# Performance work log

Hardware: AMD Instinct MI355X
Metric: run time of the kernel (lower is better)

The kernel has to match this reference:

```python
import jax, jax.numpy as jnp
import numpy as np

NO_LANE = 90  # sentinel label meaning 'no lane'

def smooth_l1(x):
    ax = jnp.abs(x)
    return jnp.where(ax < 1.0, 0.5 * x * x, ax - 0.5)

def setup_inputs() -> dict:
    key = jax.random.key(0)
    ks = jax.random.split(key, 10)
    B, M, T, L, NL, P = 32768, 6, 30, 10, 10, 50
    cls_ = jax.random.normal(ks[0], (B, M), dtype=jnp.float32)
    reg = jax.random.normal(ks[1], (B, M, T, 2), dtype=jnp.float32) * 5.0
    lane_cls = jax.random.normal(ks[2], (B, L), dtype=jnp.float32)
    gt_preds = jax.random.normal(ks[3], (B, T, 2), dtype=jnp.float32) * 5.0
    rot = jax.random.normal(ks[4], (B, 2, 2), dtype=jnp.float32)
    orig = jax.random.normal(ks[5], (B, 2), dtype=jnp.float32)
    lane_feats = jax.random.normal(ks[6], (B, NL, P, 2), dtype=jnp.float32) * 5.0
    has_preds = jax.random.uniform(ks[7], (B, T)) < 0.8
    has_preds = has_preds.at[:, 0].set(True)  # ensure mask = max_last > 1.0 holds for every row
    lane_labels = jax.random.randint(ks[8], (B,), 0, L, dtype=jnp.int32)
    lane_labels = jnp.where(jax.random.uniform(ks[9], (B,)) < 0.05, NO_LANE, lane_labels)
    return dict(cls=cls_, reg=reg, lane_cls=lane_cls, gt_preds=gt_preds, rot=rot,
                orig=orig, lane_feats=lane_feats, has_preds=has_preds, lane_labels=lane_labels)

def reference(cls, reg, lane_cls, gt_preds, rot, orig, lane_feats, has_preds, lane_labels):
    B, M, T, _ = reg.shape
    rows = jnp.arange(B)
    hasf = has_preds.astype(jnp.float32)

    # last valid timestep per agent (argmax of has + tiny time ramp)
    last = hasf + 0.1 * jnp.arange(T, dtype=jnp.float32) / T
    last_idcs = jnp.argmax(last, axis=1)
    mask = jnp.max(last, axis=1) > 1.0  # [B], all True by construction
    maskf = mask.astype(jnp.float32)

    # endpoint distance per mode -> min mode selection
    end_reg = reg[rows, :, last_idcs]            # [B, M, 2]
    end_gt = gt_preds[rows, last_idcs]           # [B, 2]
    dist = jnp.sqrt(((end_reg - end_gt[:, None, :]) ** 2).sum(-1))  # [B, M]
    min_idcs = jnp.argmin(dist, axis=1)

    # classification target: mode with min total squared error
    cls_tar = jnp.argmin(((reg - gt_preds[:, None]) ** 2).sum(-1).sum(-1), axis=1)
    nll = -jnp.take_along_axis(jax.nn.log_softmax(cls, axis=-1), cls_tar[:, None], axis=1)[:, 0]
    cls_loss = (nll * maskf).sum() / jnp.maximum(maskf.sum(), 1.0)  # CE mean over masked rows

    reg_sel = reg[rows, min_idcs]                # [B, T, 2]
    w_reg = hasf * maskf[:, None]
    reg_loss = (smooth_l1(reg_sel - gt_preds) * w_reg[:, :, None]).sum()
    num_reg = w_reg.sum()

    # lane classification: per-sample CE * (label+1), skipping sentinel
    valid = lane_labels != NO_LANE
    validf = valid.astype(jnp.float32)
    lab_c = jnp.where(valid, lane_labels, 0)
    lane_nll = -jnp.take_along_axis(jax.nn.log_softmax(lane_cls, axis=-1), lab_c[:, None], axis=1)[:, 0]
    lane_cls_loss = (lane_nll * (lab_c.astype(jnp.float32) + 1.0) * validf).sum()
    num_lane_cls = validf.sum()

    # lane-offset loss: lane polyline in global frame, point-to-lane min distances
    lane_sel = lane_feats[rows, lab_c]           # [B, P, 2]
    lane_w = jnp.einsum('bpc,bcd->bpd', lane_sel, rot) + orig[:, None, :]
    d_reg = jnp.linalg.norm(lane_w[:, None, :, :] - reg_sel[:, :, None, :], axis=-1).min(-1)  # [B, T]
    d_gt = jnp.linalg.norm(lane_w[:, None, :, :] - gt_preds[:, :, None, :], axis=-1).min(-1)  # [B, T]
    diff = d_reg - d_gt
    check = (d_reg >= d_gt).astype(jnp.float32)
    per = (diff * check * hasf).sum(1) / jnp.maximum(hasf.sum(1), 1.0)  # mean over valid steps
    w_off = validf * maskf
    lane_off_loss = (per * w_off).sum()
    num_lane_off = w_off.sum()

    return jnp.stack([cls_loss, maskf.sum() * 0 + 1.0, reg_loss, num_reg,
                      lane_cls_loss, num_lane_cls, lane_off_loss, num_lane_off])
```

## Files before the change

### kernel.cpp

```cpp
#include <hip/hip_runtime.h>
#include <math.h>

#define NO_LANE 90
constexpr int Bt  = 32768;
constexpr int Mm  = 6;
constexpr int Tt  = 30;
constexpr int Ll  = 10;
constexpr int NLl = 10;
constexpr int Pp  = 50;

constexpr int BPB   = 8;
constexpr int NBLK  = Bt / BPB;
constexpr int NSLOT = 64;

constexpr int RPAD = 368;
constexpr int GPAD = 64;
constexpr int LPAD = 104;

__device__ __forceinline__ float smoothl1(float x) {
    float ax = fabsf(x);
    return ax < 1.0f ? 0.5f * x * x : ax - 0.5f;
}

__global__ __launch_bounds__(256) void pred_loss_main(
    const float* __restrict__ cls, const float* __restrict__ reg,
    const float* __restrict__ lane_cls, const float* __restrict__ gt,
    const float* __restrict__ rot, const float* __restrict__ orig,
    const float* __restrict__ lane_feats, const unsigned char* __restrict__ hp,
    const int* __restrict__ lane_labels, float* __restrict__ slots) {

    __shared__ __align__(16) float sReg[BPB][RPAD];
    __shared__ __align__(16) float sGt[BPB][GPAD];
    __shared__ __align__(16) float sLW[BPB][LPAD];
    __shared__ float sPart[BPB][8];

    const int tid = threadIdx.x;
    const int sb  = tid >> 5;
    const int l   = tid & 31;
    const int h   = (tid >> 5) & 1;
    const int b   = blockIdx.x * BPB + sb;

    unsigned int u = ((const unsigned int*)hp)[tid & 63];
    unsigned int s = (u & 0xFFu) + ((u >> 8) & 0xFFu) +
                     ((u >> 16) & 0xFFu) + (u >> 24);
#pragma unroll
    for (int o = 32; o; o >>= 1) s += __shfl_xor((int)s, o);
    const bool byte_fmt = (s > 100u && s < 2000u);

    bool has = false;
    if (l < Tt) {
        int idx = b * Tt + l;
        has = byte_fmt ? (hp[idx] != 0)
                       : (((const unsigned int*)hp)[idx] != 0u);
    }
    unsigned long long ball = __ballot(has);
    unsigned int mmask = (unsigned int)(ball >> (h * 32));
    int   last  = 31 - __clz((int)(mmask | 1u));
    float maskf = (mmask >> 1) ? 1.0f : 0.0f;
    float n_has = (float)__popc((int)mmask);
    float hasf  = has ? 1.0f : 0.0f;

    int   lab    = lane_labels[b];
    bool  valid  = (lab != NO_LANE);
    int   lab_c  = valid ? lab : 0;
    float validf = valid ? 1.0f : 0.0f;

    const float4* regv = (const float4*)(reg + (size_t)b * (Mm * Tt * 2));
    float4* sRegV = (float4*)&sReg[sb][0];
    sRegV[l]      = regv[l];
    sRegV[l + 32] = regv[l + 32];
    if (l < 26) sRegV[l + 64] = regv[l + 64];
    if (l < 15)
        ((float4*)&sGt[sb][0])[l] = ((const float4*)(gt + (size_t)b * (Tt * 2)))[l];

    float4 R = *(const float4*)(rot + (size_t)b * 4);
    float2 O = *(const float2*)(orig + (size_t)b * 2);
    if (l < 25) {
        float4 ls = ((const float4*)(lane_feats +
                     ((size_t)b * NLl + lab_c) * (Pp * 2)))[l];
        float4 lw;
        lw.x = ls.x * R.x + ls.y * R.z + O.x;
        lw.y = ls.x * R.y + ls.y * R.w + O.y;
        lw.z = ls.z * R.x + ls.w * R.z + O.x;
        lw.w = ls.z * R.y + ls.w * R.w + O.y;
        ((float4*)&sLW[sb][0])[l] = lw;
    }

    float cm = (l < Mm) ? cls[(size_t)b * Mm + l] : -INFINITY;
    float lc = (l < Ll) ? lane_cls[(size_t)b * Ll + l] : -INFINITY;

    __syncthreads();

    float pm[Mm];
#pragma unroll
    for (int m = 0; m < Mm; ++m) pm[m] = 0.f;
    float gx = 0.f, gy = 0.f;
    if (l < Tt) {
        gx = sGt[sb][2 * l];
        gy = sGt[sb][2 * l + 1];
#pragma unroll
        for (int m = 0; m < Mm; ++m) {
            float dx = sReg[sb][m * 60 + 2 * l] - gx;
            float dy = sReg[sb][m * 60 + 2 * l + 1] - gy;
            pm[m] = dx * dx + dy * dy;
        }
    }
#pragma unroll
    for (int m = 0; m < Mm; ++m)
#pragma unroll
        for (int o = 16; o; o >>= 1) pm[m] += __shfl_xor(pm[m], o);
    int cls_tar = 0;
    float bestc = pm[0];
#pragma unroll
    for (int m = 1; m < Mm; ++m)
        if (pm[m] < bestc) { bestc = pm[m]; cls_tar = m; }

    float egx = sGt[sb][2 * last], egy = sGt[sb][2 * last + 1];
    int   min_i = 0;
    float bd = INFINITY;
#pragma unroll
    for (int m = 0; m < Mm; ++m) {
        float dx = sReg[sb][m * 60 + 2 * last] - egx;
        float dy = sReg[sb][m * 60 + 2 * last + 1] - egy;
        float d2 = dx * dx + dy * dy;
        if (d2 < bd) { bd = d2; min_i = m; }
    }

    float mx = cm;
#pragma unroll
    for (int o = 4; o; o >>= 1) mx = fmaxf(mx, __shfl_xor(mx, o));
    float ex = (l < Mm) ? __expf(cm - mx) : 0.f;
#pragma unroll
    for (int o = 4; o; o >>= 1) ex += __shfl_xor(ex, o);
    float ctar = __shfl(cm, cls_tar + h * 32);
    float nll  = mx + __logf(ex) - ctar;

    float mx2 = lc;
#pragma unroll
    for (int o = 8; o; o >>= 1) mx2 = fmaxf(mx2, __shfl_xor(mx2, o));
    float ex2 = (l < Ll) ? __expf(lc - mx2) : 0.f;
#pragma unroll
    for (int o = 8; o; o >>= 1) ex2 += __shfl_xor(ex2, o);
    float ltar = __shfl(lc, lab_c + h * 32);
    float lnll = mx2 + __logf(ex2) - ltar;

    float regl = 0.f;
    float rsx = 0.f, rsy = 0.f;
    if (l < Tt) {
        rsx = sReg[sb][min_i * 60 + 2 * l];
        rsy = sReg[sb][min_i * 60 + 2 * l + 1];
        regl = (smoothl1(rsx - gx) + smoothl1(rsy - gy)) * hasf * maskf;
    }
#pragma unroll
    for (int o = 16; o; o >>= 1) regl += __shfl_xor(regl, o);

    float dminR = INFINITY, dminG = INFINITY;
    const float4* lw4 = (const float4*)&sLW[sb][0];
#pragma unroll
    for (int j = 0; j < 25; ++j) {
        float4 q = lw4[j];
        float ax0 = q.x - rsx, ay0 = q.y - rsy;
        float ax1 = q.z - rsx, ay1 = q.w - rsy;
        dminR = fminf(dminR, fminf(ax0 * ax0 + ay0 * ay0, ax1 * ax1 + ay1 * ay1));
        float bx0 = q.x - gx, by0 = q.y - gy;
        float bx1 = q.z - gx, by1 = q.w - gy;
        dminG = fminf(dminG, fminf(bx0 * bx0 + by0 * by0, bx1 * bx1 + by1 * by1));
    }
    float pern = 0.f;
    if (l < Tt) {
        float dr = sqrtf(dminR), dg = sqrtf(dminG);
        pern = (dr >= dg) ? (dr - dg) * hasf : 0.f;
    }
#pragma unroll
    for (int o = 16; o; o >>= 1) pern += __shfl_xor(pern, o);

    if (l == 0) {
        float per = pern / fmaxf(n_has, 1.0f);
        sPart[sb][0] = nll * maskf;
        sPart[sb][1] = maskf;
        sPart[sb][2] = regl;
        sPart[sb][3] = maskf * n_has;
        sPart[sb][4] = lnll * (float)(lab_c + 1) * validf;
        sPart[sb][5] = validf;
        sPart[sb][6] = per * validf * maskf;
        sPart[sb][7] = validf * maskf;
    }
    __syncthreads();

    if (tid < 8) {
        float sum = 0.f;
#pragma unroll
        for (int k = 0; k < BPB; ++k) sum += sPart[k][tid];
        atomicAdd(&slots[(size_t)(blockIdx.x & (NSLOT - 1)) * 16 + tid], sum);
    }
}

__global__ __launch_bounds__(64) void finalize_k(const float* __restrict__ slots,
                                                 float* __restrict__ out) {
    int lane = threadIdx.x;
    int c  = lane & 7;
    int s0 = lane >> 3;
    float t = 0.f;
#pragma unroll
    for (int k = 0; k < 8; ++k)
        t += slots[(size_t)(s0 + k * 8) * 16 + c];
    t += __shfl_xor(t, 8);
    t += __shfl_xor(t, 16);
    t += __shfl_xor(t, 32);
    float r1 = __shfl(t, 1);
    if (lane == 0)      out[0] = t / fmaxf(r1, 1.0f);
    else if (lane == 1) out[1] = 1.0f;
    else if (lane < 8)  out[lane] = t;
}

extern "C" void kernel_launch(void* const* d_in, const int* in_sizes, int n_in,
                              void* d_out, int out_size, void* d_ws, size_t ws_size,
                              hipStream_t stream) {
    const float* cls        = (const float*)d_in[0];
    const float* reg        = (const float*)d_in[1];
    const float* lane_cls   = (const float*)d_in[2];
    const float* gt         = (const float*)d_in[3];
    const float* rot        = (const float*)d_in[4];
    const float* orig       = (const float*)d_in[5];
    const float* lane_feats = (const float*)d_in[6];
    const unsigned char* hp = (const unsigned char*)d_in[7];
    const int* lane_labels  = (const int*)d_in[8];
    float* out = (float*)d_out;

    float* slots = (float*)((char*)d_ws + 64);

    hipMemsetAsync(d_ws, 0, 64 + NSLOT * 16 * sizeof(float), stream);
    pred_loss_main<<<NBLK, 256, 0, stream>>>(
        cls, reg, lane_cls, gt, rot, orig, lane_feats, hp, lane_labels, slots);
    finalize_k<<<1, 64, 0, stream>>>(slots, out);
}
```

Before: 228.6 us.

## Load reg/gt into registers, use DPP reductions, fuse finalize via last-block counter

Each lane now loads its own timestep's reg and gt values straight into registers instead of staging them through shared memory. This removes a __syncthreads and the LDS traffic, and the endpoint min-mode is picked with a shuffle from lane 'last'. The small softmax and row reductions switch to DPP intrinsics in place of xor shuffles. The separate finalize kernel is folded into the main kernel with an atomic block counter, so the last block performs the final reduction, saving one launch at the cost of a threadfence and an extra atomic per block.

Measured after the change: 571.6 us. +150.1%, slower.

```diff
diff --git a/kernel.cpp b/kernel.cpp
--- a/kernel.cpp
+++ b/kernel.cpp
@@ -12,14 +12,43 @@
 constexpr int BPB   = 8;
 constexpr int NBLK  = Bt / BPB;
 constexpr int NSLOT = 64;
-
-constexpr int RPAD = 368;
-constexpr int GPAD = 64;
-constexpr int LPAD = 104;
+constexpr int LPAD  = 104;
 
 __device__ __forceinline__ float smoothl1(float x) {
     float ax = fabsf(x);
     return ax < 1.0f ? 0.5f * x * x : ax - 0.5f;
+}
+
+template <int CTRL>
+__device__ __forceinline__ float dppf(float x) {
+    return __int_as_float(__builtin_amdgcn_update_dpp(
+        0, __float_as_int(x), CTRL, 0xF, 0xF, true));
+}
+__device__ __forceinline__ float sum8(float x) {
+    x += dppf<0xB1>(x);
+    x += dppf<0x4E>(x);
+    x += dppf<0x141>(x);
+    return x;
+}
+__device__ __forceinline__ float sum16(float x) {
+    x = sum8(x);
+    x += dppf<0x140>(x);
+    return x;
+}
+__device__ __forceinline__ float sum32(float x) {
+    x += __shfl_xor(x, 16);
+    return sum16(x);
+}
+__device__ __forceinline__ float max8(float x) {
+    x = fmaxf(x, dppf<0xB1>(x));
+    x = fmaxf(x, dppf<0x4E>(x));
+    x = fmaxf(x, dppf<0x141>(x));
+    return x;
+}
+__device__ __forceinline__ float max16(float x) {
+    x = max8(x);
+    x = fmaxf(x, dppf<0x140>(x));
+    return x;
 }
 
 __global__ __launch_bounds__(256) void pred_loss_main(
@@ -27,12 +56,12 @@
     const float* __restrict__ lane_cls, const float* __restrict__ gt,
     const float* __restrict__ rot, const float* __restrict__ orig,
     const float* __restrict__ lane_feats, const unsigned char* __restrict__ hp,
-    const int* __restrict__ lane_labels, float* __restrict__ slots) {
-
-    __shared__ __align__(16) float sReg[BPB][RPAD];
-    __shared__ __align__(16) float sGt[BPB][GPAD];
+    const int* __restrict__ lane_labels, unsigned int* __restrict__ counter,
+    float* __restrict__ slots, float* __restrict__ out) {
+
     __shared__ __align__(16) float sLW[BPB][LPAD];
     __shared__ float sPart[BPB][8];
+    __shared__ int lastFlag;
 
     const int tid = threadIdx.x;
     const int sb  = tid >> 5;
@@ -65,13 +94,20 @@
     int   lab_c  = valid ? lab : 0;
     float validf = valid ? 1.0f : 0.0f;
 
-    const float4* regv = (const float4*)(reg + (size_t)b * (Mm * Tt * 2));
-    float4* sRegV = (float4*)&sReg[sb][0];
-    sRegV[l]      = regv[l];
-    sRegV[l + 32] = regv[l + 32];
-    if (l < 26) sRegV[l + 64] = regv[l + 64];
-    if (l < 15)
-        ((float4*)&sGt[sb][0])[l] = ((const float4*)(gt + (size_t)b * (Tt * 2)))[l];
+    float gx = 0.f, gy = 0.f;
+    float rx[Mm], ry[Mm];
+#pragma unroll
+    for (int m = 0; m < Mm; ++m) { rx[m] = 0.f; ry[m] = 0.f; }
+    if (l < Tt) {
+        float2 g = *(const float2*)(gt + (size_t)b * (Tt * 2) + 2 * l);
+        gx = g.x; gy = g.y;
+        const float* regb = reg + (size_t)b * (Mm * Tt * 2) + 2 * l;
+#pragma unroll
+        for (int m = 0; m < Mm; ++m) {
+            float2 r = *(const float2*)(regb + m * (Tt * 2));
+            rx[m] = r.x; ry[m] = r.y;
+        }
+    }
 
     float4 R = *(const float4*)(rot + (size_t)b * 4);
     float2 O = *(const float2*)(orig + (size_t)b * 2);
@@ -89,70 +125,47 @@
     float cm = (l < Mm) ? cls[(size_t)b * Mm + l] : -INFINITY;
     float lc = (l < Ll) ? lane_cls[(size_t)b * Ll + l] : -INFINITY;
 
-    __syncthreads();
-
     float pm[Mm];
 #pragma unroll
-    for (int m = 0; m < Mm; ++m) pm[m] = 0.f;
-    float gx = 0.f, gy = 0.f;
-    if (l < Tt) {
-        gx = sGt[sb][2 * l];
-        gy = sGt[sb][2 * l + 1];
-#pragma unroll
-        for (int m = 0; m < Mm; ++m) {
-            float dx = sReg[sb][m * 60 + 2 * l] - gx;
-            float dy = sReg[sb][m * 60 + 2 * l + 1] - gy;
-            pm[m] = dx * dx + dy * dy;
-        }
-    }
-#pragma unroll
-    for (int m = 0; m < Mm; ++m)
-#pragma unroll
-        for (int o = 16; o; o >>= 1) pm[m] += __shfl_xor(pm[m], o);
+    for (int m = 0; m < Mm; ++m) {
+        float dx = rx[m] - gx, dy = ry[m] - gy;
+        pm[m] = sum32(dx * dx + dy * dy);
+    }
     int cls_tar = 0;
     float bestc = pm[0];
 #pragma unroll
     for (int m = 1; m < Mm; ++m)
         if (pm[m] < bestc) { bestc = pm[m]; cls_tar = m; }
 
-    float egx = sGt[sb][2 * last], egy = sGt[sb][2 * last + 1];
-    int   min_i = 0;
-    float bd = INFINITY;
-#pragma unroll
-    for (int m = 0; m < Mm; ++m) {
-        float dx = sReg[sb][m * 60 + 2 * last] - egx;
-        float dy = sReg[sb][m * 60 + 2 * last + 1] - egy;
-        float d2 = dx * dx + dy * dy;
-        if (d2 < bd) { bd = d2; min_i = m; }
-    }
-
-    float mx = cm;
-#pragma unroll
-    for (int o = 4; o; o >>= 1) mx = fmaxf(mx, __shfl_xor(mx, o));
-    float ex = (l < Mm) ? __expf(cm - mx) : 0.f;
-#pragma unroll
-    for (int o = 4; o; o >>= 1) ex += __shfl_xor(ex, o);
+    int mi_loc = 0;
+    {
+        float dx = rx[0] - gx, dy = ry[0] - gy;
+        float bd = dx * dx + dy * dy;
+#pragma unroll
+        for (int m = 1; m < Mm; ++m) {
+            float ex_ = rx[m] - gx, ey_ = ry[m] - gy;
+            float d2 = ex_ * ex_ + ey_ * ey_;
+            if (d2 < bd) { bd = d2; mi_loc = m; }
+        }
+    }
+    int min_i = __shfl(mi_loc, last + h * 32);
+
+    float rsx = rx[0], rsy = ry[0];
+#pragma unroll
+    for (int m = 1; m < Mm; ++m)
+        if (min_i == m) { rsx = rx[m]; rsy = ry[m]; }
+
+    float mx = max8(cm);
+    float ex = sum8((l < Mm) ? __expf(cm - mx) : 0.f);
     float ctar = __shfl(cm, cls_tar + h * 32);
     float nll  = mx + __logf(ex) - ctar;
 
-    float mx2 = lc;
-#pragma unroll
-    for (int o = 8; o; o >>= 1) mx2 = fmaxf(mx2, __shfl_xor(mx2, o));
-    float ex2 = (l < Ll) ? __expf(lc - mx2) : 0.f;
-#pragma unroll
-    for (int o = 8; o; o >>= 1) ex2 += __shfl_xor(ex2, o);
+    float mx2 = max16(lc);
+    float ex2 = sum16((l < Ll) ? __expf(lc - mx2) : 0.f);
     float ltar = __shfl(lc, lab_c + h * 32);
     float lnll = mx2 + __logf(ex2) - ltar;
 
-    float regl = 0.f;
-    float rsx = 0.f, rsy = 0.f;
-    if (l < Tt) {
-        rsx = sReg[sb][min_i * 60 + 2 * l];
-        rsy = sReg[sb][min_i * 60 + 2 * l + 1];
-        regl = (smoothl1(rsx - gx) + smoothl1(rsy - gy)) * hasf * maskf;
-    }
-#pragma unroll
-    for (int o = 16; o; o >>= 1) regl += __shfl_xor(regl, o);
+    float regl = sum32((smoothl1(rsx - gx) + smoothl1(rsy - gy)) * hasf * maskf);
 
     float dminR = INFINITY, dminG = INFINITY;
     const float4* lw4 = (const float4*)&sLW[sb][0];
@@ -166,13 +179,8 @@
         float bx1 = q.z - gx, by1 = q.w - gy;
         dminG = fminf(dminG, fminf(bx0 * bx0 + by0 * by0, bx1 * bx1 + by1 * by1));
     }
-    float pern = 0.f;
-    if (l < Tt) {
-        float dr = sqrtf(dminR), dg = sqrtf(dminG);
-        pern = (dr >= dg) ? (dr - dg) * hasf : 0.f;
-    }
-#pragma unroll
-    for (int o = 16; o; o >>= 1) pern += __shfl_xor(pern, o);
+    float dr = sqrtf(dminR), dg = sqrtf(dminG);
+    float pern = sum32((dr >= dg) ? (dr - dg) * hasf : 0.f);
 
     if (l == 0) {
         float per = pern / fmaxf(n_has, 1.0f);
@@ -193,24 +201,30 @@
         for (int k = 0; k < BPB; ++k) sum += sPart[k][tid];
         atomicAdd(&slots[(size_t)(blockIdx.x & (NSLOT - 1)) * 16 + tid], sum);
     }
-}
-
-__global__ __launch_bounds__(64) void finalize_k(const float* __restrict__ slots,
-                                                 float* __restrict__ out) {
-    int lane = threadIdx.x;
-    int c  = lane & 7;
-    int s0 = lane >> 3;
-    float t = 0.f;
-#pragma unroll
-    for (int k = 0; k < 8; ++k)
-        t += slots[(size_t)(s0 + k * 8) * 16 + c];
-    t += __shfl_xor(t, 8);
-    t += __shfl_xor(t, 16);
-    t += __shfl_xor(t, 32);
-    float r1 = __shfl(t, 1);
-    if (lane == 0)      out[0] = t / fmaxf(r1, 1.0f);
-    else if (lane == 1) out[1] = 1.0f;
-    else if (lane < 8)  out[lane] = t;
+    __threadfence();
+    if (tid == 0) {
+        unsigned int old = atomicAdd(counter, 1u);
+        lastFlag = (old == (unsigned int)(NBLK - 1)) ? 1 : 0;
+    }
+    __syncthreads();
+
+    if (lastFlag && tid < 64) {
+        __threadfence();
+        int c  = tid & 7;
+        int s0 = tid >> 3;
+        float t = 0.f;
+#pragma unroll
+        for (int k = 0; k < 8; ++k)
+            t += __hip_atomic_load(&slots[(size_t)(s0 + k * 8) * 16 + c],
+                                   __ATOMIC_RELAXED, __HIP_MEMORY_SCOPE_AGENT);
+        t += __shfl_xor(t, 8);
+        t += __shfl_xor(t, 16);
+        t += __shfl_xor(t, 32);
+        float r1 = __shfl(t, 1);
+        if (tid == 0)      out[0] = t / fmaxf(r1, 1.0f);
+        else if (tid == 1) out[1] = 1.0f;
+        else if (tid < 8)  out[tid] = t;
+    }
 }
 
 extern "C" void kernel_launch(void* const* d_in, const int* in_sizes, int n_in,
@@ -227,10 +241,11 @@
     const int* lane_labels  = (const int*)d_in[8];
     float* out = (float*)d_out;
 
+    unsigned int* counter = (unsigned int*)d_ws;
     float* slots = (float*)((char*)d_ws + 64);
 
     hipMemsetAsync(d_ws, 0, 64 + NSLOT * 16 * sizeof(float), stream);
     pred_loss_main<<<NBLK, 256, 0, stream>>>(
-        cls, reg, lane_cls, gt, rot, orig, lane_feats, hp, lane_labels, slots);
-    finalize_k<<<1, 64, 0, stream>>>(slots, out);
-}
+        cls, reg, lane_cls, gt, rot, orig, lane_feats, hp, lane_labels,
+        counter, slots, out);
+}
```
